# Kernel optimization log

Hardware: AMD Instinct MI355X
Metric: run time of the kernel (lower is better)

Reference implementation:

```python
import jax, jax.numpy as jnp
import numpy as np

HEADS = 4
HEAD_DIM = 32
DIM = 256
HIDDEN = HEADS * HEAD_DIM  # 128
SCALE = HEAD_DIM ** -0.5


def rmsnorm(x, g):
    # channel-wise L2 normalize (dim=1) * g * sqrt(C), lucidrains-style RMSNorm for conv maps
    inv = jax.lax.rsqrt(jnp.sum(x * x, axis=1, keepdims=True) + 1e-12)
    return x * inv * (g * (x.shape[1] ** 0.5))[None, :, None, None]


def setup_inputs() -> dict:
    key = jax.random.key(0)
    k1, k2, k3 = jax.random.split(key, 3)
    b, H, W = 16, 64, 64
    x = jax.random.normal(k1, (b, DIM, H, W), dtype=jnp.float32)
    W_qkv = jax.random.normal(k2, (3 * HIDDEN, DIM), dtype=jnp.float32) * (DIM ** -0.5)
    W_out = jax.random.normal(k3, (DIM, HIDDEN), dtype=jnp.float32) * (HIDDEN ** -0.5)
    b_out = jnp.zeros((DIM,), dtype=jnp.float32)
    g_norm = jnp.ones((DIM,), dtype=jnp.float32)
    g_out = jnp.ones((DIM,), dtype=jnp.float32)
    return {"x": x, "W_qkv": W_qkv, "W_out": W_out, "b_out": b_out,
            "g_norm": g_norm, "g_out": g_out}


def reference(x, W_qkv, W_out, b_out, g_norm, g_out):
    b, c, H, W = x.shape
    n = H * W
    xn = rmsnorm(x, g_norm)
    # 1x1 conv projection to q,k,v: (b, 3*hidden, H, W)
    qkv = jnp.einsum('bchw,oc->bohw', xn, W_qkv)
    qkv = qkv.reshape(b, 3, HEADS, HEAD_DIM, n)
    q, k, v = qkv[:, 0], qkv[:, 1], qkv[:, 2]  # (b, h, d, n)
    q = jax.nn.softmax(q, axis=-2)  # over head_dim
    k = jax.nn.softmax(k, axis=-1)  # over tokens
    # context: (b, h, d, e)
    context = jnp.einsum('bhdn,bhen->bhde', k, v)
    out = jnp.einsum('bhde,bhdn->bhen', context, q) * SCALE  # (b, h, e, n)
    out = out.reshape(b, HIDDEN, H, W)
    out = jnp.einsum('bchw,oc->bohw', out, W_out) + b_out[None, :, None, None]
    return rmsnorm(out, g_out)
```

## Files before the change

### kernel.cpp

```cpp
#include <hip/hip_runtime.h>


typedef _Float16 half8 __attribute__((ext_vector_type(8)));
typedef _Float16 half4 __attribute__((ext_vector_type(4)));
typedef float f32x4 __attribute__((ext_vector_type(4)));

#define SCALE_F 0.17677669529663687f

#define GLOAD16(g, s) __builtin_amdgcn_global_load_lds( \
    (const __attribute__((address_space(1))) void*)(g), \
    (__attribute__((address_space(3))) void*)(s), 16, 0, 0)

__global__ __launch_bounds__(256) void k1_prep(const float* __restrict__ x,
                                               const float* __restrict__ g_norm,
                                               const float* __restrict__ W_qkv,
                                               const float* __restrict__ W_out,
                                               _Float16* __restrict__ W16,
                                               _Float16* __restrict__ Wo16,
                                               float* __restrict__ zbase,
                                               _Float16* __restrict__ x_t) {
  const int t = threadIdx.x;
  if (blockIdx.x == 64) {
    #pragma unroll
    for (int i = 0; i < 8; ++i) {
      int idx = blockIdx.y * 2048 + i * 256 + t;
      f32x4 v;
      if (idx < 24576) v = *(const f32x4*)(W_qkv + (size_t)idx * 4);
      else             v = *(const f32x4*)(W_out + (size_t)(idx - 24576) * 4);
      half4 h = {(_Float16)v[0], (_Float16)v[1], (_Float16)v[2], (_Float16)v[3]};
      if (idx < 24576) *(half4*)(W16 + (size_t)idx * 4) = h;
      else             *(half4*)(Wo16 + (size_t)(idx - 24576) * 4) = h;
    }
    return;
  }
  if (blockIdx.x == 65) {
    const f32x4 fz = {0.f, 0.f, 0.f, 0.f};
    float* zb = zbase + blockIdx.y * 4224;
    for (int off = t * 4; off < 4224; off += 1024)
      *(f32x4*)(zb + off) = fz;
    return;
  }
  const int b = blockIdx.y;
  const int p0 = blockIdx.x * 64;
  __shared__ _Float16 tile[256][68];
  __shared__ float g16s[256];
  __shared__ float psum[64][4];
  __shared__ float sinv[64];
  g16s[t] = g_norm[t] * 16.0f;
  const float* xb = x + (size_t)b * 256 * 4096;
  #pragma unroll
  for (int it = 0; it < 16; ++it) {
    int c = it * 16 + (t >> 4);
    int px = (t & 15) * 4;
    f32x4 v = *(const f32x4*)(xb + (size_t)c * 4096 + p0 + px);
    half4 h = {(_Float16)v[0], (_Float16)v[1], (_Float16)v[2], (_Float16)v[3]};
    *(half4*)&tile[c][px] = h;
  }
  __syncthreads();
  {
    int px = t & 63, q = t >> 6;
    float s = 0.f;
    #pragma unroll
    for (int i = 0; i < 64; ++i) {
      float f = (float)tile[q * 64 + i][px];
      s += f * f;
    }
    psum[px][q] = s;
  }
  __syncthreads();
  if (t < 64) {
    float s = psum[t][0] + psum[t][1] + psum[t][2] + psum[t][3];
    sinv[t] = rsqrtf(s + 1e-12f);
  }
  __syncthreads();
  _Float16* xt = x_t + ((size_t)b * 4096 + p0) * 256;
  #pragma unroll
  for (int j = 0; j < 8; ++j) {
    int idx8 = t + 256 * j;
    int px = idx8 >> 5;
    int c8 = (idx8 & 31) * 8;
    float iv = sinv[px];
    half8 h;
    #pragma unroll
    for (int i = 0; i < 8; ++i)
      h[i] = (_Float16)((float)tile[c8 + i][px] * iv * g16s[c8 + i]);
    *(half8*)(xt + (size_t)px * 256 + c8) = h;
  }
}

__global__ __launch_bounds__(256, 2) void k2_fused(const _Float16* __restrict__ W16,
                                                   const _Float16* __restrict__ x_t,
                                                   _Float16* __restrict__ qhat,
                                                   float* __restrict__ ctx,
                                                   float* __restrict__ sumexp) {
  const int pt = blockIdx.x, b = blockIdx.y;
  const int p0 = pt * 128;
  const int t = threadIdx.x;
  const int wid = t >> 6, l = t & 63;
  const int wm = (wid >> 1) << 6, wn = (wid & 1) << 6;
  __shared__ __align__(1024) char smem[65536];
  float* rp = (float*)smem;
  _Float16* vbuf = (_Float16*)(smem + 17408);
  char* wtile = smem + 32768;
  const _Float16* Xbase = x_t + ((size_t)b * 4096 + p0) * 256;
  _Float16* qb = qhat + ((size_t)b * 4096 + p0) * 128;
  const f32x4 fz = {0.f, 0.f, 0.f, 0.f};
  #pragma unroll
  for (int mt = 0; mt < 3; ++mt) {
    f32x4 acc[4][4];
    #pragma unroll
    for (int i = 0; i < 4; ++i)
      #pragma unroll
      for (int j = 0; j < 4; ++j) acc[i][j] = fz;
    const _Float16* Wmt = W16 + (size_t)(mt * 128) * 256;
    for (int kt = 0; kt < 4; ++kt) {
      #pragma unroll
      for (int i = 0; i < 4; ++i) {
        int q = ((wid * 4 + i) << 6) + l;
        int r = q >> 3, s = q & 7;
        int co = kt * 64 + ((s ^ (r & 7)) << 3);
        GLOAD16(Wmt + (size_t)r * 256 + co, smem + ((wid * 4 + i) << 10));
        GLOAD16(Xbase + (size_t)r * 256 + co, smem + 16384 + ((wid * 4 + i) << 10));
      }
      __syncthreads();
      #pragma unroll
      for (int kk = 0; kk < 2; ++kk) {
        half8 af[4], bf[4];
        int ck = kk * 4 + (l >> 4);
        #pragma unroll
        for (int mf = 0; mf < 4; ++mf) {
          int r = wm + mf * 16 + (l & 15);
          af[mf] = *(const half8*)(smem + r * 128 + ((ck ^ (r & 7)) << 4));
        }
        #pragma unroll
        for (int nf = 0; nf < 4; ++nf) {
          int r = wn + nf * 16 + (l & 15);
          bf[nf] = *(const half8*)(smem + 16384 + r * 128 + ((ck ^ (r & 7)) << 4));
        }
        #pragma unroll
        for (int mf = 0; mf < 4; ++mf)
          #pragma unroll
          for (int nf = 0; nf < 4; ++nf)
            acc[mf][nf] = __builtin_amdgcn_mfma_f32_16x16x32_f16(af[mf], bf[nf], acc[mf][nf], 0, 0, 0);
      }
      __syncthreads();
    }
    #pragma unroll
    for (int qi = 0; qi < 4; ++qi) {
      if ((wid >> 1) == (qi >> 1)) {
        const int mfb = (qi & 1) << 1;
        #pragma unroll
        for (int mo = 0; mo < 2; ++mo)
          #pragma unroll
          for (int nf = 0; nf < 4; ++nf)
            #pragma unroll
            for (int rr = 0; rr < 4; ++rr)
              rp[(mo * 16 + (l >> 4) * 4 + rr) * 132 + wn + nf * 16 + (l & 15)] =
                  acc[mfb + mo][nf][rr];
      }
      __syncthreads();
      if (mt == 0) {
        int px = t & 127, hf = t >> 7;
        float w[32];
        float ssum = 0.f;
        #pragma unroll
        for (int i = 0; i < 32; ++i) { w[i] = __expf(rp[i * 132 + px]); ssum += w[i]; }
        float inv = 1.0f / ssum;
        if (hf == 0) {
          #pragma unroll
          for (int i = 0; i < 16; ++i) vbuf[i * 128 + px] = (_Float16)(w[i] * inv);
        } else {
          #pragma unroll
          for (int i = 0; i < 16; ++i) vbuf[(16 + i) * 128 + px] = (_Float16)(w[16 + i] * inv);
        }
        __syncthreads();
        #pragma unroll
        for (int i = 0; i < 2; ++i) {
          int ci = t + 256 * i;
          int px2 = ci >> 2, c8 = (ci & 3) * 8;
          half8 h;
          #pragma unroll
          for (int j = 0; j < 8; ++j) h[j] = vbuf[(c8 + j) * 128 + px2];
          *(half8*)(qb + (size_t)px2 * 128 + qi * 32 + c8) = h;
        }
      } else if (mt == 1) {
        #pragma unroll
        for (int i = 0; i < 2; ++i) {
          int ci = t + 256 * i;
          int c = ci >> 4, s = ci & 15;
          const float* rr_ = &rp[c * 132 + s * 8];
          float sm = 0.f;
          half8 h;
          #pragma unroll
          for (int j = 0; j < 8; ++j) {
            float e = __expf(rr_[j] - 10.f);
            sm += e;
            h[j] = (_Float16)e;
          }
          int gc = qi * 32 + c;
          *(half8*)(wtile + gc * 256 + ((s ^ (gc & 15)) << 4)) = h;
          sm += __shfl_xor(sm, 1);
          sm += __shfl_xor(sm, 2);
          sm += __shfl_xor(sm, 4);
          sm += __shfl_xor(sm, 8);
          if ((l & 15) == 0) atomicAdd(&sumexp[b * 128 + gc], sm);
        }
        __syncthreads();
      } else {
        #pragma unroll
        for (int i = 0; i < 2; ++i) {
          int ci = t + 256 * i;
          int c = ci >> 4, s = ci & 15;
          const float* rr_ = &rp[c * 132 + s * 8];
          half8 h;
          #pragma unroll
          for (int j = 0; j < 8; ++j) h[j] = (_Float16)rr_[j];
          *(half8*)((char*)vbuf + c * 256 + ((s ^ (c & 15)) << 4)) = h;
        }
        __syncthreads();
        if (wid == qi) {
          f32x4 ca[2][2] = {{fz, fz}, {fz, fz}};
          #pragma unroll
          for (int kk = 0; kk < 4; ++kk) {
            half8 a2[2], b2[2];
            int sl = kk * 4 + (l >> 4);
            #pragma unroll
            for (int ti = 0; ti < 2; ++ti) {
              int gc = qi * 32 + ti * 16 + (l & 15);
              a2[ti] = *(const half8*)(wtile + gc * 256 + ((sl ^ (gc & 15)) << 4));
              int lc = ti * 16 + (l & 15);
              b2[ti] = *(const half8*)((char*)vbuf + lc * 256 + ((sl ^ (lc & 15)) << 4));
            }
            #pragma unroll
            for (int ti = 0; ti < 2; ++ti)
              #pragma unroll
              for (int tj = 0; tj < 2; ++tj)
                ca[ti][tj] = __builtin_amdgcn_mfma_f32_16x16x32_f16(a2[ti], b2[tj], ca[ti][tj], 0, 0, 0);
          }
          float* cb = ctx + (size_t)(b * 4 + qi) * 1024;
          #pragma unroll
          for (int ti = 0; ti < 2; ++ti)
            #pragma unroll
            for (int tj = 0; tj < 2; ++tj)
              #pragma unroll
              for (int rr = 0; rr < 4; ++rr)
                atomicAdd(&cb[(ti * 16 + (l >> 4) * 4 + rr) * 32 + tj * 16 + (l & 15)],
                          ca[ti][tj][rr]);
        }
      }
    }
    if (mt < 2) __syncthreads();
  }
}

__global__ __launch_bounds__(256) void k4b_fold(const _Float16* __restrict__ Wo16,
                                                const float* __restrict__ ctx,
                                                const float* __restrict__ sumexp,
                                                _Float16* __restrict__ M) {
  const int mq = blockIdx.x, b = blockIdx.y;
  const int t = threadIdx.x;
  const int h = t >> 6, l = t & 63;
  const int m0 = mq * 64;
  const float* cb = ctx + (size_t)(b * 4 + h) * 1024;
  const float* sb = sumexp + b * 128 + h * 32;
  half8 bf[2];
  #pragma unroll
  for (int n0 = 0; n0 < 2; ++n0) {
    int d = n0 * 16 + (l & 15);
    float s = SCALE_F / sb[d];
    const float* ce = cb + d * 32 + (l >> 4) * 8;
    half8 hb;
    #pragma unroll
    for (int j = 0; j < 8; ++j) hb[j] = (_Float16)(ce[j] * s);
    bf[n0] = hb;
  }
  const f32x4 fz = {0.f, 0.f, 0.f, 0.f};
  _Float16* Mb = M + (size_t)(b * 256) * 128;
  #pragma unroll
  for (int mf = 0; mf < 4; ++mf) {
    int row = m0 + mf * 16 + (l & 15);
    half8 af = *(const half8*)(Wo16 + (size_t)row * 128 + h * 32 + (l >> 4) * 8);
    #pragma unroll
    for (int n0 = 0; n0 < 2; ++n0) {
      f32x4 c = __builtin_amdgcn_mfma_f32_16x16x32_f16(af, bf[n0], fz, 0, 0, 0);
      #pragma unroll
      for (int rr = 0; rr < 4; ++rr) {
        int r = m0 + mf * 16 + (l >> 4) * 4 + rr;
        Mb[(size_t)r * 128 + h * 32 + n0 * 16 + (l & 15)] = (_Float16)c[rr];
      }
    }
  }
}

__global__ __launch_bounds__(256) void k5c_out(const _Float16* __restrict__ M,
                                               const _Float16* __restrict__ qhat,
                                               const float* __restrict__ b_out,
                                               const float* __restrict__ g_out,
                                               float* __restrict__ out) {
  const int pt = blockIdx.x, b = blockIdx.y;
  const int p0 = pt * 64;
  const int t = threadIdx.x;
  const int wid = t >> 6, l = t & 63;
  __shared__ __align__(16) char smem[81920];
  float* rp = (float*)smem;
  float* bo = (float*)(smem + 69632);
  float* g16o = (float*)(smem + 70656);
  float* psum = (float*)(smem + 71680);
  float* sinvp = (float*)(smem + 72704);
  const _Float16* Mb = M + (size_t)b * 256 * 128;
  const _Float16* Qb = qhat + ((size_t)b * 4096 + p0) * 128;
  #pragma unroll
  for (int i = 0; i < 16; ++i) {
    int ci = t + 256 * i;
    int r = ci >> 4, c = ci & 15;
    *(half8*)(smem + r * 256 + ((c ^ (r & 15)) << 4)) = *(const half8*)(Mb + (size_t)r * 128 + c * 8);
  }
  #pragma unroll
  for (int i = 0; i < 4; ++i) {
    int ci = t + 256 * i;
    int r = ci >> 4, c = ci & 15;
    *(half8*)(smem + 65536 + r * 256 + ((c ^ (r & 15)) << 4)) = *(const half8*)(Qb + (size_t)r * 128 + c * 8);
  }
  __syncthreads();
  const f32x4 fz = {0.f, 0.f, 0.f, 0.f};
  f32x4 acc[4][4];
  #pragma unroll
  for (int i = 0; i < 4; ++i)
    #pragma unroll
    for (int j = 0; j < 4; ++j) acc[i][j] = fz;
  #pragma unroll
  for (int kk = 0; kk < 4; ++kk) {
    half8 af[4], bf[4];
    int ck = kk * 4 + (l >> 4);
    #pragma unroll
    for (int mf = 0; mf < 4; ++mf) {
      int r = wid * 64 + mf * 16 + (l & 15);
      af[mf] = *(const half8*)(smem + r * 256 + ((ck ^ (r & 15)) << 4));
    }
    #pragma unroll
    for (int nf = 0; nf < 4; ++nf) {
      int r = nf * 16 + (l & 15);
      bf[nf] = *(const half8*)(smem + 65536 + r * 256 + ((ck ^ (r & 15)) << 4));
    }
    #pragma unroll
    for (int mf = 0; mf < 4; ++mf)
      #pragma unroll
      for (int nf = 0; nf < 4; ++nf)
        acc[mf][nf] = __builtin_amdgcn_mfma_f32_16x16x32_f16(af[mf], bf[nf], acc[mf][nf], 0, 0, 0);
  }
  __syncthreads();
  bo[t] = b_out[t];
  g16o[t] = g_out[t] * 16.0f;
  #pragma unroll
  for (int mf = 0; mf < 4; ++mf)
    #pragma unroll
    for (int nf = 0; nf < 4; ++nf)
      #pragma unroll
      for (int rr = 0; rr < 4; ++rr) {
        int r = wid * 64 + mf * 16 + (l >> 4) * 4 + rr;
        int px = nf * 16 + (l & 15);
        rp[r * 68 + px] = acc[mf][nf][rr];
      }
  __syncthreads();
  {
    int px = t & 63, q = t >> 6;
    float s = 0.f;
    #pragma unroll
    for (int i = 0; i < 64; ++i) {
      int r = q * 64 + i;
      float f = rp[r * 68 + px] + bo[r];
      s += f * f;
    }
    psum[px * 4 + q] = s;
  }
  __syncthreads();
  if (t < 64)
    sinvp[t] = rsqrtf(psum[t * 4] + psum[t * 4 + 1] + psum[t * 4 + 2] + psum[t * 4 + 3] + 1e-12f);
  __syncthreads();
  float* ob = out + (size_t)(b * 256) * 4096 + p0;
  #pragma unroll
  for (int i = 0; i < 16; ++i) {
    int idx4 = t + 256 * i;
    int r = idx4 >> 4, px4 = (idx4 & 15) * 4;
    f32x4 v;
    #pragma unroll
    for (int ii = 0; ii < 4; ++ii)
      v[ii] = (rp[r * 68 + px4 + ii] + bo[r]) * sinvp[px4 + ii] * g16o[r];
    *(f32x4*)(ob + (size_t)r * 4096 + px4) = v;
  }
}

extern "C" void kernel_launch(void* const* d_in, const int* in_sizes, int n_in,
                              void* d_out, int out_size, void* d_ws, size_t ws_size,
                              hipStream_t stream) {
  const float* x      = (const float*)d_in[0];
  const float* W_qkv  = (const float*)d_in[1];
  const float* W_out  = (const float*)d_in[2];
  const float* b_out  = (const float*)d_in[3];
  const float* g_norm = (const float*)d_in[4];
  const float* g_out  = (const float*)d_in[5];
  float* out = (float*)d_out;
  char* ws = (char*)d_ws;
  if (ws_size < 51912704) return;

  _Float16* W16  = (_Float16*)(ws);
  _Float16* x_t  = (_Float16*)(ws + 196608);
  _Float16* qhat = (_Float16*)(ws + 33751040);
  float*    ctx  = (float*)(ws + 50528256);
  float*    sume = (float*)(ws + 50790400);
  _Float16* M    = (_Float16*)(ws + 50798592);
  _Float16* Wo16 = (_Float16*)(ws + 51847168);

  k1_prep<<<dim3(66, 16), 256, 0, stream>>>(x, g_norm, W_qkv, W_out, W16, Wo16, ctx, x_t);
  k2_fused<<<dim3(32, 16), 256, 0, stream>>>(W16, x_t, qhat, ctx, sume);
  k4b_fold<<<dim3(4, 16), 256, 0, stream>>>(Wo16, ctx, sume, M);
  k5c_out<<<dim3(64, 16), 256, 0, stream>>>(M, qhat, b_out, g_out, out);
}
```

Before: 88.10 us.

## Restructure QKV kernel: per-wave head ownership with register-resident softmax and context

The fused QKV/softmax/context kernel now uses 64-pixel tiles with the full X tile loaded once into LDS, and each wave owns one head. Weights are read straight from global memory into registers. Softmaxes are computed from MFMA accumulators using lane shuffles rather than via an LDS staging round-trip with many block barriers. This cuts synchronisation and LDS traffic and doubles the grid, at the cost of uncached global weight reads per wave, more ctx atomics, and higher LDS usage (76KB), which may limit occupancy.

```diff
diff --git a/kernel.cpp b/kernel.cpp
--- a/kernel.cpp
+++ b/kernel.cpp
@@ -94,162 +94,167 @@
                                                    float* __restrict__ ctx,
                                                    float* __restrict__ sumexp) {
   const int pt = blockIdx.x, b = blockIdx.y;
-  const int p0 = pt * 128;
+  const int p0 = pt * 64;
   const int t = threadIdx.x;
-  const int wid = t >> 6, l = t & 63;
-  const int wm = (wid >> 1) << 6, wn = (wid & 1) << 6;
-  __shared__ __align__(1024) char smem[65536];
-  float* rp = (float*)smem;
-  _Float16* vbuf = (_Float16*)(smem + 17408);
-  char* wtile = smem + 32768;
+  const int w = t >> 6, l = t & 63;
+  const int lg = l >> 4, ll = l & 15;
+  __shared__ __align__(1024) char smem[77824];
+  char* xbuf = smem;
+  char* wt = smem + 32768 + w * 5632;
+  char* vt = smem + 55296 + w * 5632;
+  _Float16* qt = (_Float16*)(smem + 55296 + w * 5632);
+
   const _Float16* Xbase = x_t + ((size_t)b * 4096 + p0) * 256;
-  _Float16* qb = qhat + ((size_t)b * 4096 + p0) * 128;
+  #pragma unroll
+  for (int i = 0; i < 8; ++i) {
+    int q = (w * 8 + i) * 64 + l;
+    int px = q >> 5, c = q & 31;
+    int cs = c ^ (px & 15);
+    GLOAD16(Xbase + (size_t)px * 256 + cs * 8, smem + (w * 8 + i) * 1024);
+  }
+  __syncthreads();
+
   const f32x4 fz = {0.f, 0.f, 0.f, 0.f};
   #pragma unroll
   for (int mt = 0; mt < 3; ++mt) {
-    f32x4 acc[4][4];
-    #pragma unroll
-    for (int i = 0; i < 4; ++i)
+    f32x4 acc[2][4];
+    #pragma unroll
+    for (int i = 0; i < 2; ++i)
       #pragma unroll
       for (int j = 0; j < 4; ++j) acc[i][j] = fz;
-    const _Float16* Wmt = W16 + (size_t)(mt * 128) * 256;
-    for (int kt = 0; kt < 4; ++kt) {
+    const _Float16* Wb = W16 + (size_t)(mt * 128 + w * 32) * 256;
+    #pragma unroll
+    for (int ks = 0; ks < 8; ++ks) {
+      half8 af[2], bf[4];
+      #pragma unroll
+      for (int mf = 0; mf < 2; ++mf)
+        af[mf] = *(const half8*)(Wb + (size_t)(mf * 16 + ll) * 256 + ks * 32 + lg * 8);
+      #pragma unroll
+      for (int nf = 0; nf < 4; ++nf) {
+        int px = nf * 16 + ll;
+        int c = (ks * 4 + lg) ^ (px & 15);
+        bf[nf] = *(const half8*)(xbuf + px * 512 + c * 16);
+      }
+      #pragma unroll
+      for (int mf = 0; mf < 2; ++mf)
+        #pragma unroll
+        for (int nf = 0; nf < 4; ++nf)
+          acc[mf][nf] = __builtin_amdgcn_mfma_f32_16x16x32_f16(af[mf], bf[nf], acc[mf][nf], 0, 0, 0);
+    }
+    if (mt == 0) {
+      float e[2][4][4];
+      float s[4] = {0.f, 0.f, 0.f, 0.f};
+      #pragma unroll
+      for (int mf = 0; mf < 2; ++mf)
+        #pragma unroll
+        for (int nf = 0; nf < 4; ++nf)
+          #pragma unroll
+          for (int rr = 0; rr < 4; ++rr) {
+            float v = __expf(acc[mf][nf][rr]);
+            e[mf][nf][rr] = v;
+            s[nf] += v;
+          }
+      #pragma unroll
+      for (int nf = 0; nf < 4; ++nf) {
+        s[nf] += __shfl_xor(s[nf], 16);
+        s[nf] += __shfl_xor(s[nf], 32);
+        s[nf] = 1.0f / s[nf];
+      }
+      #pragma unroll
+      for (int mf = 0; mf < 2; ++mf)
+        #pragma unroll
+        for (int nf = 0; nf < 4; ++nf) {
+          half4 h;
+          #pragma unroll
+          for (int rr = 0; rr < 4; ++rr) h[rr] = (_Float16)(e[mf][nf][rr] * s[nf]);
+          *(half4*)(qt + (nf * 16 + ll) * 40 + mf * 16 + lg * 4) = h;
+        }
+      __syncthreads();
       #pragma unroll
       for (int i = 0; i < 4; ++i) {
-        int q = ((wid * 4 + i) << 6) + l;
-        int r = q >> 3, s = q & 7;
-        int co = kt * 64 + ((s ^ (r & 7)) << 3);
-        GLOAD16(Wmt + (size_t)r * 256 + co, smem + ((wid * 4 + i) << 10));
-        GLOAD16(Xbase + (size_t)r * 256 + co, smem + 16384 + ((wid * 4 + i) << 10));
-      }
+        int q = i * 64 + l;
+        int px = q >> 2, c8 = (q & 3) * 8;
+        half8 h = *(const half8*)(qt + px * 40 + c8);
+        *(half8*)(qhat + ((size_t)b * 4096 + p0 + px) * 128 + w * 32 + c8) = h;
+      }
+    } else if (mt == 1) {
+      float e[2][4][4];
+      float rs[2][4];
+      #pragma unroll
+      for (int mf = 0; mf < 2; ++mf)
+        #pragma unroll
+        for (int rr = 0; rr < 4; ++rr) rs[mf][rr] = 0.f;
+      #pragma unroll
+      for (int mf = 0; mf < 2; ++mf)
+        #pragma unroll
+        for (int nf = 0; nf < 4; ++nf)
+          #pragma unroll
+          for (int rr = 0; rr < 4; ++rr) {
+            float v = __expf(acc[mf][nf][rr] - 10.f);
+            e[mf][nf][rr] = v;
+            rs[mf][rr] += v;
+          }
+      #pragma unroll
+      for (int mf = 0; mf < 2; ++mf)
+        #pragma unroll
+        for (int rr = 0; rr < 4; ++rr) {
+          float v = rs[mf][rr];
+          v += __shfl_xor(v, 1);
+          v += __shfl_xor(v, 2);
+          v += __shfl_xor(v, 4);
+          v += __shfl_xor(v, 8);
+          rs[mf][rr] = v;
+        }
+      if (ll == 0) {
+        #pragma unroll
+        for (int mf = 0; mf < 2; ++mf)
+          #pragma unroll
+          for (int rr = 0; rr < 4; ++rr)
+            atomicAdd(&sumexp[b * 128 + w * 32 + mf * 16 + lg * 4 + rr], rs[mf][rr]);
+      }
+      #pragma unroll
+      for (int mf = 0; mf < 2; ++mf)
+        #pragma unroll
+        for (int nf = 0; nf < 4; ++nf)
+          #pragma unroll
+          for (int rr = 0; rr < 4; ++rr)
+            *(_Float16*)(wt + (mf * 16 + lg * 4 + rr) * 176 + (nf * 16 + ll) * 2) =
+                (_Float16)e[mf][nf][rr];
       __syncthreads();
+    } else {
+      #pragma unroll
+      for (int mf = 0; mf < 2; ++mf)
+        #pragma unroll
+        for (int nf = 0; nf < 4; ++nf)
+          #pragma unroll
+          for (int rr = 0; rr < 4; ++rr)
+            *(_Float16*)(vt + (mf * 16 + lg * 4 + rr) * 176 + (nf * 16 + ll) * 2) =
+                (_Float16)acc[mf][nf][rr];
+      __syncthreads();
+      f32x4 ca[2][2] = {{fz, fz}, {fz, fz}};
       #pragma unroll
       for (int kk = 0; kk < 2; ++kk) {
-        half8 af[4], bf[4];
-        int ck = kk * 4 + (l >> 4);
-        #pragma unroll
-        for (int mf = 0; mf < 4; ++mf) {
-          int r = wm + mf * 16 + (l & 15);
-          af[mf] = *(const half8*)(smem + r * 128 + ((ck ^ (r & 7)) << 4));
+        half8 a2[2], b2[2];
+        #pragma unroll
+        for (int ti = 0; ti < 2; ++ti) {
+          a2[ti] = *(const half8*)(wt + (ti * 16 + ll) * 176 + kk * 64 + lg * 16);
+          b2[ti] = *(const half8*)(vt + (ti * 16 + ll) * 176 + kk * 64 + lg * 16);
         }
         #pragma unroll
-        for (int nf = 0; nf < 4; ++nf) {
-          int r = wn + nf * 16 + (l & 15);
-          bf[nf] = *(const half8*)(smem + 16384 + r * 128 + ((ck ^ (r & 7)) << 4));
-        }
-        #pragma unroll
-        for (int mf = 0; mf < 4; ++mf)
-          #pragma unroll
-          for (int nf = 0; nf < 4; ++nf)
-            acc[mf][nf] = __builtin_amdgcn_mfma_f32_16x16x32_f16(af[mf], bf[nf], acc[mf][nf], 0, 0, 0);
-      }
-      __syncthreads();
-    }
-    #pragma unroll
-    for (int qi = 0; qi < 4; ++qi) {
-      if ((wid >> 1) == (qi >> 1)) {
-        const int mfb = (qi & 1) << 1;
-        #pragma unroll
-        for (int mo = 0; mo < 2; ++mo)
-          #pragma unroll
-          for (int nf = 0; nf < 4; ++nf)
-            #pragma unroll
-            for (int rr = 0; rr < 4; ++rr)
-              rp[(mo * 16 + (l >> 4) * 4 + rr) * 132 + wn + nf * 16 + (l & 15)] =
-                  acc[mfb + mo][nf][rr];
-      }
-      __syncthreads();
-      if (mt == 0) {
-        int px = t & 127, hf = t >> 7;
-        float w[32];
-        float ssum = 0.f;
-        #pragma unroll
-        for (int i = 0; i < 32; ++i) { w[i] = __expf(rp[i * 132 + px]); ssum += w[i]; }
-        float inv = 1.0f / ssum;
-        if (hf == 0) {
-          #pragma unroll
-          for (int i = 0; i < 16; ++i) vbuf[i * 128 + px] = (_Float16)(w[i] * inv);
-        } else {
-          #pragma unroll
-          for (int i = 0; i < 16; ++i) vbuf[(16 + i) * 128 + px] = (_Float16)(w[16 + i] * inv);
-        }
-        __syncthreads();
-        #pragma unroll
-        for (int i = 0; i < 2; ++i) {
-          int ci = t + 256 * i;
-          int px2 = ci >> 2, c8 = (ci & 3) * 8;
-          half8 h;
-          #pragma unroll
-          for (int j = 0; j < 8; ++j) h[j] = vbuf[(c8 + j) * 128 + px2];
-          *(half8*)(qb + (size_t)px2 * 128 + qi * 32 + c8) = h;
-        }
-      } else if (mt == 1) {
-        #pragma unroll
-        for (int i = 0; i < 2; ++i) {
-          int ci = t + 256 * i;
-          int c = ci >> 4, s = ci & 15;
-          const float* rr_ = &rp[c * 132 + s * 8];
-          float sm = 0.f;
-          half8 h;
-          #pragma unroll
-          for (int j = 0; j < 8; ++j) {
-            float e = __expf(rr_[j] - 10.f);
-            sm += e;
-            h[j] = (_Float16)e;
-          }
-          int gc = qi * 32 + c;
-          *(half8*)(wtile + gc * 256 + ((s ^ (gc & 15)) << 4)) = h;
-          sm += __shfl_xor(sm, 1);
-          sm += __shfl_xor(sm, 2);
-          sm += __shfl_xor(sm, 4);
-          sm += __shfl_xor(sm, 8);
-          if ((l & 15) == 0) atomicAdd(&sumexp[b * 128 + gc], sm);
-        }
-        __syncthreads();
-      } else {
-        #pragma unroll
-        for (int i = 0; i < 2; ++i) {
-          int ci = t + 256 * i;
-          int c = ci >> 4, s = ci & 15;
-          const float* rr_ = &rp[c * 132 + s * 8];
-          half8 h;
-          #pragma unroll
-          for (int j = 0; j < 8; ++j) h[j] = (_Float16)rr_[j];
-          *(half8*)((char*)vbuf + c * 256 + ((s ^ (c & 15)) << 4)) = h;
-        }
-        __syncthreads();
-        if (wid == qi) {
-          f32x4 ca[2][2] = {{fz, fz}, {fz, fz}};
-          #pragma unroll
-          for (int kk = 0; kk < 4; ++kk) {
-            half8 a2[2], b2[2];
-            int sl = kk * 4 + (l >> 4);
-            #pragma unroll
-            for (int ti = 0; ti < 2; ++ti) {
-              int gc = qi * 32 + ti * 16 + (l & 15);
-              a2[ti] = *(const half8*)(wtile + gc * 256 + ((sl ^ (gc & 15)) << 4));
-              int lc = ti * 16 + (l & 15);
-              b2[ti] = *(const half8*)((char*)vbuf + lc * 256 + ((sl ^ (lc & 15)) << 4));
-            }
-            #pragma unroll
-            for (int ti = 0; ti < 2; ++ti)
-              #pragma unroll
-              for (int tj = 0; tj < 2; ++tj)
-                ca[ti][tj] = __builtin_amdgcn_mfma_f32_16x16x32_f16(a2[ti], b2[tj], ca[ti][tj], 0, 0, 0);
-          }
-          float* cb = ctx + (size_t)(b * 4 + qi) * 1024;
-          #pragma unroll
-          for (int ti = 0; ti < 2; ++ti)
-            #pragma unroll
-            for (int tj = 0; tj < 2; ++tj)
-              #pragma unroll
-              for (int rr = 0; rr < 4; ++rr)
-                atomicAdd(&cb[(ti * 16 + (l >> 4) * 4 + rr) * 32 + tj * 16 + (l & 15)],
-                          ca[ti][tj][rr]);
-        }
-      }
-    }
-    if (mt < 2) __syncthreads();
+        for (int ti = 0; ti < 2; ++ti)
+          #pragma unroll
+          for (int tj = 0; tj < 2; ++tj)
+            ca[ti][tj] = __builtin_amdgcn_mfma_f32_16x16x32_f16(a2[ti], b2[tj], ca[ti][tj], 0, 0, 0);
+      }
+      float* cb = ctx + (size_t)(b * 4 + w) * 1024;
+      #pragma unroll
+      for (int ti = 0; ti < 2; ++ti)
+        #pragma unroll
+        for (int tj = 0; tj < 2; ++tj)
+          #pragma unroll
+          for (int rr = 0; rr < 4; ++rr)
+            atomicAdd(&cb[(ti * 16 + lg * 4 + rr) * 32 + tj * 16 + ll], ca[ti][tj][rr]);
+    }
   }
 }
 
@@ -412,7 +417,7 @@
   _Float16* Wo16 = (_Float16*)(ws + 51847168);
 
   k1_prep<<<dim3(66, 16), 256, 0, stream>>>(x, g_norm, W_qkv, W_out, W16, Wo16, ctx, x_t);
-  k2_fused<<<dim3(32, 16), 256, 0, stream>>>(W16, x_t, qhat, ctx, sume);
+  k2_fused<<<dim3(64, 16), 256, 0, stream>>>(W16, x_t, qhat, ctx, sume);
   k4b_fold<<<dim3(4, 16), 256, 0, stream>>>(Wo16, ctx, sume, M);
   k5c_out<<<dim3(64, 16), 256, 0, stream>>>(M, qhat, b_out, g_out, out);
 }
```

Result: slower. 97.96 us (+11.2%).
